# Performance work log

Hardware: AMD Instinct MI355X
Metric: run time of the kernel (lower is better)

## Reference

```python
import jax, jax.numpy as jnp
import numpy as np

C = 64   # input_channels
H = 128  # hidden_channels


def setup_inputs() -> dict:
    key = jax.random.key(0)
    ks = jax.random.split(key, 13)
    s = lambda k, shape, fan_in: jax.random.uniform(k, shape, jnp.float32, -1.0, 1.0) / np.sqrt(fan_in)
    return {
        "x": jax.random.normal(ks[0], (2, 512, C), jnp.float32),
        "Wa": s(ks[1], (C, H), C),  "ba": s(ks[2], (H,), C),
        "Wb": s(ks[3], (H, H), H), "bb": s(ks[4], (H,), H),
        "Wc1": s(ks[5], (H, H), H), "bc1": s(ks[6], (H,), H),
        "Wc2": s(ks[7], (H, H), H), "bc2": s(ks[8], (H,), H),
        "Wc3": s(ks[9], (H, H), H), "bc3": s(ks[10], (H,), H),
        "Wo": s(ks[11], (H, 1), H), "bo": s(ks[12], (1,), H),
    }


def reference(x, Wa, ba, Wb, bb, Wc1, bc1, Wc2, bc2, Wc3, bc3, Wo, bo):
    B, N, _ = x.shape
    # node MLP
    h = jax.nn.relu(jnp.einsum("bnc,ch->bnh", x, Wa) + ba)
    h = jax.nn.relu(jnp.einsum("bnh,hk->bnk", h, Wb) + bb)
    # pairwise difference: diff[b,i,j] = h[b,j] - h[b,i]  (matches x_a - x_b)
    d = h[:, None, :, :] - h[:, :, None, :]  # [B,N,N,H]
    e = jax.nn.relu(jnp.einsum("bijh,hk->bijk", d, Wc1) + bc1)
    e = jax.nn.relu(jnp.einsum("bijh,hk->bijk", e, Wc2) + bc2)
    e = jax.nn.relu(jnp.einsum("bijh,hk->bijk", e, Wc3) + bc3)
    out = jnp.einsum("bijh,ho->bijo", e, Wo) + bo  # [B,N,N,1]
    return out[..., 0]  # [B,N,N]
```

## Files before the change

### kernel.cpp

```cpp
#include <hip/hip_runtime.h>


typedef _Float16 half_t;
typedef __attribute__((ext_vector_type(2))) _Float16 f16x2;
typedef __attribute__((ext_vector_type(8))) _Float16 f16x8;
typedef __attribute__((ext_vector_type(4))) float f32x4;


__global__ __launch_bounds__(256) void prep_kernel(
    const float* __restrict__ x, const float* __restrict__ Wa, const float* __restrict__ ba,
    const float* __restrict__ Wb, const float* __restrict__ bb, const float* __restrict__ Wc1,
    const float* __restrict__ bc1, const float* __restrict__ Wc2, const float* __restrict__ Wc3,
    half_t* __restrict__ gh, half_t* __restrict__ gbh,
    half_t* __restrict__ W2T, half_t* __restrict__ W3T)
{
  const int t = threadIdx.x;
  if (blockIdx.x >= 256) {
    const int bid = blockIdx.x - 256;
    const int layer = bid >> 3, nt = bid & 7;
    const int ks = t >> 6, L = t & 63, q = L >> 4, cc = L & 15;
    const float* src = layer ? Wc3 : Wc2;
    half_t* dst = layer ? W3T : W2T;
    f16x8 v;
    #pragma unroll
    for (int e = 0; e < 8; e++)
      v[e] = (half_t)src[(32 * ks + 8 * q + e) * 128 + 16 * nt + cc];
    *(f16x8*)(dst + (ks * 8 + nt) * 512 + L * 8) = v;
    return;
  }
  __shared__ float sx[64 * 6];
  __shared__ float sh1[128 * 6];
  __shared__ float sh2[128 * 6];
  const int n0 = blockIdx.x * 4;
  const int col = t & 127, hf = t >> 7;

  sx[(t & 63) * 6 + (t >> 6)] = x[(n0 + (t >> 6)) * 64 + (t & 63)];
  __syncthreads();

  float a0 = ba[col], a1 = a0;
  #pragma unroll
  for (int cc = 0; cc < 64; cc++) {
    const float wv = Wa[cc * 128 + col];
    const float2 xv = *(const float2*)(sx + cc * 6 + hf * 2);
    a0 = fmaf(xv.x, wv, a0); a1 = fmaf(xv.y, wv, a1);
  }
  *(float2*)(sh1 + col * 6 + hf * 2) = make_float2(fmaxf(a0, 0.f), fmaxf(a1, 0.f));
  __syncthreads();

  float b0 = bb[col], b1 = b0;
  #pragma unroll
  for (int k = 0; k < 128; k++) {
    const float wv = Wb[k * 128 + col];
    const float2 hv = *(const float2*)(sh1 + k * 6 + hf * 2);
    b0 = fmaf(hv.x, wv, b0); b1 = fmaf(hv.y, wv, b1);
  }
  *(float2*)(sh2 + col * 6 + hf * 2) = make_float2(fmaxf(b0, 0.f), fmaxf(b1, 0.f));
  __syncthreads();

  float c0 = 0.f, c1 = 0.f;
  #pragma unroll
  for (int k = 0; k < 128; k++) {
    const float wv = Wc1[k * 128 + col];
    const float2 hv = *(const float2*)(sh2 + k * 6 + hf * 2);
    c0 = fmaf(hv.x, wv, c0); c1 = fmaf(hv.y, wv, c1);
  }
  const float bv = bc1[col];
  const int r0 = n0 + hf * 2;
  gh [(r0 + 0) * 128 + col] = (half_t)c0;
  gh [(r0 + 1) * 128 + col] = (half_t)c1;
  gbh[(r0 + 0) * 128 + col] = (half_t)(c0 + bv);
  gbh[(r0 + 1) * 128 + col] = (half_t)(c1 + bv);
}

static __device__ inline f16x8 relu_sub8(f16x8 a, f16x8 b) {
  f16x8 d = a - b;
  const f16x8 z = {};
  return __builtin_elementwise_max(d, z);
}

__global__ __launch_bounds__(256)
void edge_kernel(
    const half_t* __restrict__ gh, const half_t* __restrict__ gbh,
    const half_t* __restrict__ W2T, const half_t* __restrict__ W3T,
    const float* __restrict__ bc2, const float* __restrict__ bc3,
    const float* __restrict__ Wo, const float* __restrict__ bo,
    float* __restrict__ out)
{
  __shared__ half_t sE[4 * 16 * 512];
  const int t = threadIdx.x, lane = t & 63, w = t >> 6;
  const int c = lane & 15, q = lane >> 4;
  const int bid = blockIdx.x;
  const int b = bid >> 8, jq = (bid >> 7) & 1, ic = bid & 127;
  const int i0 = ic * 4;
  const int j0w = jq * 256 + w * 64;

  half_t* sEw = sE + w * (16 * 512);
  const float bo0 = bo[0];
  const int packoff = ((q >> 1) * 16 + c) * 8 + (q & 1) * 4;
  const int rdoff = lane * 8;

  for (int u = 0; u < 4; u++) {
    const int i = i0 + u;

    f16x8 e1[4][4];
    {
      f16x8 gih[4];
      #pragma unroll
      for (int ks = 0; ks < 4; ks++)
        gih[ks] = *(const f16x8*)(gh + (size_t)(b * 512 + i) * 128 + ks * 32 + q * 8);
      #pragma unroll
      for (int ks = 0; ks < 4; ks++)
        #pragma unroll
        for (int jt = 0; jt < 4; jt++) {
          const f16x8 gj = *(const f16x8*)(gbh + (size_t)(b * 512 + j0w + jt * 16 + c) * 128 + ks * 32 + q * 8);
          e1[ks][jt] = relu_sub8(gj, gih[ks]);
        }
    }

    #pragma unroll 1
    for (int nt = 0; nt < 8; nt++) {
      f16x8 wf[4];
      #pragma unroll
      for (int ks = 0; ks < 4; ks++)
        wf[ks] = *(const f16x8*)(W2T + (ks * 8 + nt) * 512 + rdoff);
      f32x4 acc[4] = {};
      #pragma unroll
      for (int ks = 0; ks < 4; ks++)
        #pragma unroll
        for (int jt = 0; jt < 4; jt++)
          acc[jt] = __builtin_amdgcn_mfma_f32_16x16x32_f16(wf[ks], e1[ks][jt], acc[jt], 0, 0, 0);
      const f32x4 b2 = *(const f32x4*)(bc2 + nt * 16 + q * 4);
      const int po = ((nt >> 1) * 512) + packoff + (nt & 1) * 256;
      #pragma unroll
      for (int jt = 0; jt < 4; jt++) {
        const f32x4 v = acc[jt];
        const float r0 = fmaxf(v[0] + b2[0], 0.f), r1 = fmaxf(v[1] + b2[1], 0.f);
        const float r2 = fmaxf(v[2] + b2[2], 0.f), r3 = fmaxf(v[3] + b2[3], 0.f);
        f16x2 h01, h23;
        h01[0] = (half_t)r0; h01[1] = (half_t)r1;
        h23[0] = (half_t)r2; h23[1] = (half_t)r3;
        uint2 uv;
        uv.x = __builtin_bit_cast(unsigned int, h01);
        uv.y = __builtin_bit_cast(unsigned int, h23);
        *(uint2*)(sEw + jt * 2048 + po) = uv;
      }
    }

    f16x8 be[4][4];
    #pragma unroll
    for (int ks3 = 0; ks3 < 4; ks3++)
      #pragma unroll
      for (int jt = 0; jt < 4; jt++)
        be[ks3][jt] = *(const f16x8*)(sEw + (jt * 4 + ks3) * 512 + rdoff);

    float p[4] = {0.f, 0.f, 0.f, 0.f};
    #pragma unroll 1
    for (int nt = 0; nt < 8; nt++) {
      f16x8 wf[4];
      #pragma unroll
      for (int ks3 = 0; ks3 < 4; ks3++)
        wf[ks3] = *(const f16x8*)(W3T + (ks3 * 8 + nt) * 512 + rdoff);
      f32x4 acc[4] = {};
      #pragma unroll
      for (int ks3 = 0; ks3 < 4; ks3++)
        #pragma unroll
        for (int jt = 0; jt < 4; jt++)
          acc[jt] = __builtin_amdgcn_mfma_f32_16x16x32_f16(wf[ks3], be[ks3][jt], acc[jt], 0, 0, 0);
      const f32x4 b3 = *(const f32x4*)(bc3 + nt * 16 + q * 4);
      const f32x4 wo = *(const f32x4*)(Wo  + nt * 16 + q * 4);
      #pragma unroll
      for (int jt = 0; jt < 4; jt++)
        #pragma unroll
        for (int r = 0; r < 4; r++)
          p[jt] = fmaf(fmaxf(acc[jt][r] + b3[r], 0.f), wo[r], p[jt]);
    }

    #pragma unroll
    for (int jt = 0; jt < 4; jt++) {
      p[jt] += __shfl_xor(p[jt], 16, 64);
      p[jt] += __shfl_xor(p[jt], 32, 64);
    }
    if (q == 0) {
      const size_t base = ((size_t)(b * 512 + i)) * 512 + j0w;
      #pragma unroll
      for (int jt = 0; jt < 4; jt++)
        out[base + jt * 16 + c] = p[jt] + bo0;
    }
  }
}

extern "C" void kernel_launch(void* const* d_in, const int* in_sizes, int n_in,
                              void* d_out, int out_size, void* d_ws, size_t ws_size,
                              hipStream_t stream)
{
  const float* x   = (const float*)d_in[0];
  const float* Wa  = (const float*)d_in[1];
  const float* ba  = (const float*)d_in[2];
  const float* Wb  = (const float*)d_in[3];
  const float* bb  = (const float*)d_in[4];
  const float* Wc1 = (const float*)d_in[5];
  const float* bc1 = (const float*)d_in[6];
  const float* Wc2 = (const float*)d_in[7];
  const float* bc2 = (const float*)d_in[8];
  const float* Wc3 = (const float*)d_in[9];
  const float* bc3 = (const float*)d_in[10];
  const float* Wo  = (const float*)d_in[11];
  const float* bo  = (const float*)d_in[12];
  float* out = (float*)d_out;

  char* ws = (char*)d_ws;
  half_t* gh  = (half_t*)ws;
  half_t* gbh = (half_t*)(ws + 262144);
  half_t* W2T = (half_t*)(ws + 524288);
  half_t* W3T = (half_t*)(ws + 557056);

  prep_kernel<<<272, 256, 0, stream>>>(x, Wa, ba, Wb, bb, Wc1, bc1, Wc2, Wc3,
                                       gh, gbh, W2T, W3T);
  edge_kernel<<<512, 256, 0, stream>>>(gh, gbh, W2T, W3T, bc2, bc3, Wo, bo, out);
}
```

Baseline: 133.0 us.

## Halve per-wave j tile, double grid, hoist gj loads, fold bias into accumulator

Each wave now handles 32 j columns instead of 64, the grid doubles to 1024 blocks, and LDS per block is halved. The launch bounds ask for 4 blocks per CU to raise occupancy. The gbh rows for j are loaded once per block and reused across the four i iterations, and the biases are used as the initial MFMA accumulator values. Weight tiles are reordered so each nt reads contiguous memory, and s_setprio brackets the MFMA bursts. The trade-off is less reuse of each weight fragment per MFMA, since only two j tiles share each wf load.

```diff
diff --git a/kernel.cpp b/kernel.cpp
--- a/kernel.cpp
+++ b/kernel.cpp
@@ -25,7 +25,7 @@
     #pragma unroll
     for (int e = 0; e < 8; e++)
       v[e] = (half_t)src[(32 * ks + 8 * q + e) * 128 + 16 * nt + cc];
-    *(f16x8*)(dst + (ks * 8 + nt) * 512 + L * 8) = v;
+    *(f16x8*)(dst + (nt * 4 + ks) * 512 + L * 8) = v;
     return;
   }
   __shared__ float sx[64 * 6];
@@ -78,7 +78,7 @@
   return __builtin_elementwise_max(d, z);
 }
 
-__global__ __launch_bounds__(256)
+__global__ __launch_bounds__(256, 4)
 void edge_kernel(
     const half_t* __restrict__ gh, const half_t* __restrict__ gbh,
     const half_t* __restrict__ W2T, const half_t* __restrict__ W3T,
@@ -86,23 +86,31 @@
     const float* __restrict__ Wo, const float* __restrict__ bo,
     float* __restrict__ out)
 {
-  __shared__ half_t sE[4 * 16 * 512];
+  __shared__ half_t sE[4 * 8 * 512];
   const int t = threadIdx.x, lane = t & 63, w = t >> 6;
   const int c = lane & 15, q = lane >> 4;
   const int bid = blockIdx.x;
-  const int b = bid >> 8, jq = (bid >> 7) & 1, ic = bid & 127;
+  const int b = bid >> 9, jq = (bid >> 7) & 3, ic = bid & 127;
   const int i0 = ic * 4;
-  const int j0w = jq * 256 + w * 64;
-
-  half_t* sEw = sE + w * (16 * 512);
+  const int j0w = jq * 128 + w * 32;
+
+  half_t* sEw = sE + w * (8 * 512);
   const float bo0 = bo[0];
   const int packoff = ((q >> 1) * 16 + c) * 8 + (q & 1) * 4;
   const int rdoff = lane * 8;
 
+  f16x8 gj[4][2];
+  #pragma unroll
+  for (int ks = 0; ks < 4; ks++)
+    #pragma unroll
+    for (int jt = 0; jt < 2; jt++)
+      gj[ks][jt] = *(const f16x8*)(gbh + (size_t)(b * 512 + j0w + jt * 16 + c) * 128 + ks * 32 + q * 8);
+
+  #pragma unroll 1
   for (int u = 0; u < 4; u++) {
     const int i = i0 + u;
 
-    f16x8 e1[4][4];
+    f16x8 e1[4][2];
     {
       f16x8 gih[4];
       #pragma unroll
@@ -111,10 +119,8 @@
       #pragma unroll
       for (int ks = 0; ks < 4; ks++)
         #pragma unroll
-        for (int jt = 0; jt < 4; jt++) {
-          const f16x8 gj = *(const f16x8*)(gbh + (size_t)(b * 512 + j0w + jt * 16 + c) * 128 + ks * 32 + q * 8);
-          e1[ks][jt] = relu_sub8(gj, gih[ks]);
-        }
+        for (int jt = 0; jt < 2; jt++)
+          e1[ks][jt] = relu_sub8(gj[ks][jt], gih[ks]);
     }
 
     #pragma unroll 1
@@ -122,23 +128,23 @@
       f16x8 wf[4];
       #pragma unroll
       for (int ks = 0; ks < 4; ks++)
-        wf[ks] = *(const f16x8*)(W2T + (ks * 8 + nt) * 512 + rdoff);
-      f32x4 acc[4] = {};
-      #pragma unroll
-      for (int ks = 0; ks < 4; ks++)
-        #pragma unroll
-        for (int jt = 0; jt < 4; jt++)
+        wf[ks] = *(const f16x8*)(W2T + nt * 2048 + ks * 512 + rdoff);
+      const f32x4 b2 = *(const f32x4*)(bc2 + nt * 16 + q * 4);
+      f32x4 acc[2] = {b2, b2};
+      __builtin_amdgcn_s_setprio(1);
+      #pragma unroll
+      for (int ks = 0; ks < 4; ks++)
+        #pragma unroll
+        for (int jt = 0; jt < 2; jt++)
           acc[jt] = __builtin_amdgcn_mfma_f32_16x16x32_f16(wf[ks], e1[ks][jt], acc[jt], 0, 0, 0);
-      const f32x4 b2 = *(const f32x4*)(bc2 + nt * 16 + q * 4);
+      __builtin_amdgcn_s_setprio(0);
       const int po = ((nt >> 1) * 512) + packoff + (nt & 1) * 256;
       #pragma unroll
-      for (int jt = 0; jt < 4; jt++) {
+      for (int jt = 0; jt < 2; jt++) {
         const f32x4 v = acc[jt];
-        const float r0 = fmaxf(v[0] + b2[0], 0.f), r1 = fmaxf(v[1] + b2[1], 0.f);
-        const float r2 = fmaxf(v[2] + b2[2], 0.f), r3 = fmaxf(v[3] + b2[3], 0.f);
         f16x2 h01, h23;
-        h01[0] = (half_t)r0; h01[1] = (half_t)r1;
-        h23[0] = (half_t)r2; h23[1] = (half_t)r3;
+        h01[0] = (half_t)fmaxf(v[0], 0.f); h01[1] = (half_t)fmaxf(v[1], 0.f);
+        h23[0] = (half_t)fmaxf(v[2], 0.f); h23[1] = (half_t)fmaxf(v[3], 0.f);
         uint2 uv;
         uv.x = __builtin_bit_cast(unsigned int, h01);
         uv.y = __builtin_bit_cast(unsigned int, h23);
@@ -146,44 +152,46 @@
       }
     }
 
-    f16x8 be[4][4];
+    f16x8 be[4][2];
     #pragma unroll
     for (int ks3 = 0; ks3 < 4; ks3++)
       #pragma unroll
-      for (int jt = 0; jt < 4; jt++)
+      for (int jt = 0; jt < 2; jt++)
         be[ks3][jt] = *(const f16x8*)(sEw + (jt * 4 + ks3) * 512 + rdoff);
 
-    float p[4] = {0.f, 0.f, 0.f, 0.f};
+    float p[2] = {0.f, 0.f};
     #pragma unroll 1
     for (int nt = 0; nt < 8; nt++) {
       f16x8 wf[4];
       #pragma unroll
       for (int ks3 = 0; ks3 < 4; ks3++)
-        wf[ks3] = *(const f16x8*)(W3T + (ks3 * 8 + nt) * 512 + rdoff);
-      f32x4 acc[4] = {};
+        wf[ks3] = *(const f16x8*)(W3T + nt * 2048 + ks3 * 512 + rdoff);
+      const f32x4 b3 = *(const f32x4*)(bc3 + nt * 16 + q * 4);
+      f32x4 acc[2] = {b3, b3};
+      __builtin_amdgcn_s_setprio(1);
       #pragma unroll
       for (int ks3 = 0; ks3 < 4; ks3++)
         #pragma unroll
-        for (int jt = 0; jt < 4; jt++)
+        for (int jt = 0; jt < 2; jt++)
           acc[jt] = __builtin_amdgcn_mfma_f32_16x16x32_f16(wf[ks3], be[ks3][jt], acc[jt], 0, 0, 0);
-      const f32x4 b3 = *(const f32x4*)(bc3 + nt * 16 + q * 4);
-      const f32x4 wo = *(const f32x4*)(Wo  + nt * 16 + q * 4);
-      #pragma unroll
-      for (int jt = 0; jt < 4; jt++)
+      __builtin_amdgcn_s_setprio(0);
+      const f32x4 wo = *(const f32x4*)(Wo + nt * 16 + q * 4);
+      #pragma unroll
+      for (int jt = 0; jt < 2; jt++)
         #pragma unroll
         for (int r = 0; r < 4; r++)
-          p[jt] = fmaf(fmaxf(acc[jt][r] + b3[r], 0.f), wo[r], p[jt]);
-    }
-
-    #pragma unroll
-    for (int jt = 0; jt < 4; jt++) {
+          p[jt] = fmaf(fmaxf(acc[jt][r], 0.f), wo[r], p[jt]);
+    }
+
+    #pragma unroll
+    for (int jt = 0; jt < 2; jt++) {
       p[jt] += __shfl_xor(p[jt], 16, 64);
       p[jt] += __shfl_xor(p[jt], 32, 64);
     }
     if (q == 0) {
       const size_t base = ((size_t)(b * 512 + i)) * 512 + j0w;
       #pragma unroll
-      for (int jt = 0; jt < 4; jt++)
+      for (int jt = 0; jt < 2; jt++)
         out[base + jt * 16 + c] = p[jt] + bo0;
     }
   }
@@ -216,5 +224,5 @@
 
   prep_kernel<<<272, 256, 0, stream>>>(x, Wa, ba, Wb, bb, Wc1, bc1, Wc2, Wc3,
                                        gh, gbh, W2T, W3T);
-  edge_kernel<<<512, 256, 0, stream>>>(gh, gbh, W2T, W3T, bc2, bc3, Wo, bo, out);
-}
+  edge_kernel<<<1024, 256, 0, stream>>>(gh, gbh, W2T, W3T, bc2, bc3, Wo, bo, out);
+}
```

Result: no change. 132.6 us (-0.2%).

## Split edge kernel into producer/consumer waves with LDS-resident weights

Applied to the files above, without the earlier changes.

The edge kernel now uses warp specialization. Two waves compute layer 2 into a double-buffered LDS tile while two other waves run layer 3 and the output projection on the previous row, so the two layers overlap. W2T and W3T are staged once per block into LDS with a new tile order, and the biases are folded into the accumulator init. Each block covers 16 rows instead of 4, which halves the grid to 256 blocks and adds a barrier per stage. The risks are lower occupancy from the roughly 130KB of LDS and fewer blocks than the MI355X has CUs.

```diff
diff --git a/kernel.cpp b/kernel.cpp
--- a/kernel.cpp
+++ b/kernel.cpp
@@ -25,7 +25,7 @@
     #pragma unroll
     for (int e = 0; e < 8; e++)
       v[e] = (half_t)src[(32 * ks + 8 * q + e) * 128 + 16 * nt + cc];
-    *(f16x8*)(dst + (ks * 8 + nt) * 512 + L * 8) = v;
+    *(f16x8*)(dst + (nt * 4 + ks) * 512 + L * 8) = v;
     return;
   }
   __shared__ float sx[64 * 6];
@@ -86,106 +86,131 @@
     const float* __restrict__ Wo, const float* __restrict__ bo,
     float* __restrict__ out)
 {
-  __shared__ half_t sE[4 * 16 * 512];
+  __shared__ __align__(16) half_t sW2[16384];
+  __shared__ __align__(16) half_t sW3[16384];
+  __shared__ __align__(16) float  sBf[384];
+  __shared__ __align__(16) half_t sE[32768];
+
   const int t = threadIdx.x, lane = t & 63, w = t >> 6;
   const int c = lane & 15, q = lane >> 4;
   const int bid = blockIdx.x;
-  const int b = bid >> 8, jq = (bid >> 7) & 1, ic = bid & 127;
-  const int i0 = ic * 4;
-  const int j0w = jq * 256 + w * 64;
-
-  half_t* sEw = sE + w * (16 * 512);
+  const int b = bid >> 7, jq = (bid >> 5) & 3, ic = bid & 31;
+  const int i0 = ic * 16;
+  const bool producer = (w < 2);
+  const int pw = producer ? w : (w - 2);
+  const int j0 = jq * 128 + pw * 64;
+
+  #pragma unroll
+  for (int k = 0; k < 8; k++) {
+    const int off = (k * 256 + t) * 8;
+    *(f16x8*)(sW2 + off) = *(const f16x8*)(W2T + off);
+    *(f16x8*)(sW3 + off) = *(const f16x8*)(W3T + off);
+  }
+  for (int s = t; s < 384; s += 256)
+    sBf[s] = (s < 128) ? bc2[s] : ((s < 256) ? bc3[s - 128] : Wo[s - 256]);
+  __syncthreads();
+
   const float bo0 = bo[0];
   const int packoff = ((q >> 1) * 16 + c) * 8 + (q & 1) * 4;
   const int rdoff = lane * 8;
 
-  for (int u = 0; u < 4; u++) {
-    const int i = i0 + u;
-
-    f16x8 e1[4][4];
-    {
-      f16x8 gih[4];
-      #pragma unroll
-      for (int ks = 0; ks < 4; ks++)
-        gih[ks] = *(const f16x8*)(gh + (size_t)(b * 512 + i) * 128 + ks * 32 + q * 8);
-      #pragma unroll
-      for (int ks = 0; ks < 4; ks++)
+  #pragma unroll 1
+  for (int r = 0; r < 17; ++r) {
+    if (producer) {
+      if (r < 16) {
+        const int i = i0 + r;
+        f16x8 e1[4][4];
+        {
+          f16x8 gih[4];
+          #pragma unroll
+          for (int ks = 0; ks < 4; ks++)
+            gih[ks] = *(const f16x8*)(gh + (size_t)(b * 512 + i) * 128 + ks * 32 + q * 8);
+          #pragma unroll
+          for (int ks = 0; ks < 4; ks++)
+            #pragma unroll
+            for (int jt = 0; jt < 4; jt++) {
+              const f16x8 gj = *(const f16x8*)(gbh + (size_t)(b * 512 + j0 + jt * 16 + c) * 128 + ks * 32 + q * 8);
+              e1[ks][jt] = relu_sub8(gj, gih[ks]);
+            }
+        }
+        half_t* sEw = sE + (pw * 2 + (r & 1)) * 8192;
+        #pragma unroll 1
+        for (int nt = 0; nt < 8; nt++) {
+          f16x8 wf[4];
+          #pragma unroll
+          for (int ks = 0; ks < 4; ks++)
+            wf[ks] = *(const f16x8*)(sW2 + (nt * 4 + ks) * 512 + rdoff);
+          const f32x4 b2 = *(const f32x4*)(sBf + nt * 16 + q * 4);
+          f32x4 acc[4] = {b2, b2, b2, b2};
+          __builtin_amdgcn_s_setprio(1);
+          #pragma unroll
+          for (int ks = 0; ks < 4; ks++)
+            #pragma unroll
+            for (int jt = 0; jt < 4; jt++)
+              acc[jt] = __builtin_amdgcn_mfma_f32_16x16x32_f16(wf[ks], e1[ks][jt], acc[jt], 0, 0, 0);
+          __builtin_amdgcn_s_setprio(0);
+          const int po = ((nt >> 1) * 512) + packoff + (nt & 1) * 256;
+          #pragma unroll
+          for (int jt = 0; jt < 4; jt++) {
+            const f32x4 v = acc[jt];
+            f16x2 h01, h23;
+            h01[0] = (half_t)fmaxf(v[0], 0.f); h01[1] = (half_t)fmaxf(v[1], 0.f);
+            h23[0] = (half_t)fmaxf(v[2], 0.f); h23[1] = (half_t)fmaxf(v[3], 0.f);
+            uint2 uv;
+            uv.x = __builtin_bit_cast(unsigned int, h01);
+            uv.y = __builtin_bit_cast(unsigned int, h23);
+            *(uint2*)(sEw + jt * 2048 + po) = uv;
+          }
+        }
+      }
+    } else {
+      if (r >= 1) {
+        const int i = i0 + r - 1;
+        const half_t* sEc = sE + (pw * 2 + ((r - 1) & 1)) * 8192;
+        f16x8 be[4][4];
+        #pragma unroll
+        for (int ks3 = 0; ks3 < 4; ks3++)
+          #pragma unroll
+          for (int jt = 0; jt < 4; jt++)
+            be[ks3][jt] = *(const f16x8*)(sEc + (jt * 4 + ks3) * 512 + rdoff);
+
+        float p[4] = {0.f, 0.f, 0.f, 0.f};
+        #pragma unroll 1
+        for (int mt = 0; mt < 8; mt++) {
+          f16x8 wf[4];
+          #pragma unroll
+          for (int ks3 = 0; ks3 < 4; ks3++)
+            wf[ks3] = *(const f16x8*)(sW3 + (mt * 4 + ks3) * 512 + rdoff);
+          const f32x4 b3 = *(const f32x4*)(sBf + 128 + mt * 16 + q * 4);
+          f32x4 acc[4] = {b3, b3, b3, b3};
+          __builtin_amdgcn_s_setprio(1);
+          #pragma unroll
+          for (int ks3 = 0; ks3 < 4; ks3++)
+            #pragma unroll
+            for (int jt = 0; jt < 4; jt++)
+              acc[jt] = __builtin_amdgcn_mfma_f32_16x16x32_f16(wf[ks3], be[ks3][jt], acc[jt], 0, 0, 0);
+          __builtin_amdgcn_s_setprio(0);
+          const f32x4 wo = *(const f32x4*)(sBf + 256 + mt * 16 + q * 4);
+          #pragma unroll
+          for (int jt = 0; jt < 4; jt++)
+            #pragma unroll
+            for (int rr = 0; rr < 4; rr++)
+              p[jt] = fmaf(fmaxf(acc[jt][rr], 0.f), wo[rr], p[jt]);
+        }
         #pragma unroll
         for (int jt = 0; jt < 4; jt++) {
-          const f16x8 gj = *(const f16x8*)(gbh + (size_t)(b * 512 + j0w + jt * 16 + c) * 128 + ks * 32 + q * 8);
-          e1[ks][jt] = relu_sub8(gj, gih[ks]);
-        }
-    }
-
-    #pragma unroll 1
-    for (int nt = 0; nt < 8; nt++) {
-      f16x8 wf[4];
-      #pragma unroll
-      for (int ks = 0; ks < 4; ks++)
-        wf[ks] = *(const f16x8*)(W2T + (ks * 8 + nt) * 512 + rdoff);
-      f32x4 acc[4] = {};
-      #pragma unroll
-      for (int ks = 0; ks < 4; ks++)
-        #pragma unroll
-        for (int jt = 0; jt < 4; jt++)
-          acc[jt] = __builtin_amdgcn_mfma_f32_16x16x32_f16(wf[ks], e1[ks][jt], acc[jt], 0, 0, 0);
-      const f32x4 b2 = *(const f32x4*)(bc2 + nt * 16 + q * 4);
-      const int po = ((nt >> 1) * 512) + packoff + (nt & 1) * 256;
-      #pragma unroll
-      for (int jt = 0; jt < 4; jt++) {
-        const f32x4 v = acc[jt];
-        const float r0 = fmaxf(v[0] + b2[0], 0.f), r1 = fmaxf(v[1] + b2[1], 0.f);
-        const float r2 = fmaxf(v[2] + b2[2], 0.f), r3 = fmaxf(v[3] + b2[3], 0.f);
-        f16x2 h01, h23;
-        h01[0] = (half_t)r0; h01[1] = (half_t)r1;
-        h23[0] = (half_t)r2; h23[1] = (half_t)r3;
-        uint2 uv;
-        uv.x = __builtin_bit_cast(unsigned int, h01);
-        uv.y = __builtin_bit_cast(unsigned int, h23);
-        *(uint2*)(sEw + jt * 2048 + po) = uv;
+          p[jt] += __shfl_xor(p[jt], 16, 64);
+          p[jt] += __shfl_xor(p[jt], 32, 64);
+        }
+        if (q == 0) {
+          const size_t base = ((size_t)(b * 512 + i)) * 512 + j0;
+          #pragma unroll
+          for (int jt = 0; jt < 4; jt++)
+            out[base + jt * 16 + c] = p[jt] + bo0;
+        }
       }
     }
-
-    f16x8 be[4][4];
-    #pragma unroll
-    for (int ks3 = 0; ks3 < 4; ks3++)
-      #pragma unroll
-      for (int jt = 0; jt < 4; jt++)
-        be[ks3][jt] = *(const f16x8*)(sEw + (jt * 4 + ks3) * 512 + rdoff);
-
-    float p[4] = {0.f, 0.f, 0.f, 0.f};
-    #pragma unroll 1
-    for (int nt = 0; nt < 8; nt++) {
-      f16x8 wf[4];
-      #pragma unroll
-      for (int ks3 = 0; ks3 < 4; ks3++)
-        wf[ks3] = *(const f16x8*)(W3T + (ks3 * 8 + nt) * 512 + rdoff);
-      f32x4 acc[4] = {};
-      #pragma unroll
-      for (int ks3 = 0; ks3 < 4; ks3++)
-        #pragma unroll
-        for (int jt = 0; jt < 4; jt++)
-          acc[jt] = __builtin_amdgcn_mfma_f32_16x16x32_f16(wf[ks3], be[ks3][jt], acc[jt], 0, 0, 0);
-      const f32x4 b3 = *(const f32x4*)(bc3 + nt * 16 + q * 4);
-      const f32x4 wo = *(const f32x4*)(Wo  + nt * 16 + q * 4);
-      #pragma unroll
-      for (int jt = 0; jt < 4; jt++)
-        #pragma unroll
-        for (int r = 0; r < 4; r++)
-          p[jt] = fmaf(fmaxf(acc[jt][r] + b3[r], 0.f), wo[r], p[jt]);
-    }
-
-    #pragma unroll
-    for (int jt = 0; jt < 4; jt++) {
-      p[jt] += __shfl_xor(p[jt], 16, 64);
-      p[jt] += __shfl_xor(p[jt], 32, 64);
-    }
-    if (q == 0) {
-      const size_t base = ((size_t)(b * 512 + i)) * 512 + j0w;
-      #pragma unroll
-      for (int jt = 0; jt < 4; jt++)
-        out[base + jt * 16 + c] = p[jt] + bo0;
-    }
+    __syncthreads();
   }
 }
 
@@ -216,5 +241,5 @@
 
   prep_kernel<<<272, 256, 0, stream>>>(x, Wa, ba, Wb, bb, Wc1, bc1, Wc2, Wc3,
                                        gh, gbh, W2T, W3T);
-  edge_kernel<<<512, 256, 0, stream>>>(gh, gbh, W2T, W3T, bc2, bc3, Wo, bo, out);
-}
+  edge_kernel<<<256, 256, 0, stream>>>(gh, gbh, W2T, W3T, bc2, bc3, Wo, bo, out);
+}
```

Result: slower. 152.0 us (+14.3%).
